# Kernel optimization log

Measured on AMD Instinct MI355X. Metric: run time of the kernel, lower is better.

The kernel has to match this reference:

```python
import jax, jax.numpy as jnp
import numpy as np
from jax import lax

# Mamba2 config (matches init_kwargs + mamba_ssm defaults)
B_SZ, SEQ = 8, 2048
D_MODEL, D_STATE, EXPAND, HEADDIM = 1024, 128, 2, 64
D_INNER = EXPAND * D_MODEL            # 2048
NHEADS = D_INNER // HEADDIM           # 32
NGROUPS, D_CONV, CHUNK = 1, 4, 128
CONV_DIM = D_INNER + 2 * NGROUPS * D_STATE
D_IN_PROJ = 2 * D_INNER + 2 * NGROUPS * D_STATE + NHEADS
VAR_NUM, EPS = 3, 1e-5


def setup_inputs() -> dict:
    key = jax.random.key(0)
    ks = jax.random.split(key, 10)
    return {
        "embed_data": jax.random.normal(ks[0], (B_SZ, SEQ, D_MODEL), jnp.float32),
        "in_proj_w": jax.random.normal(ks[1], (D_IN_PROJ, D_MODEL), jnp.float32) * 0.02,
        "conv_w": jax.random.normal(ks[2], (CONV_DIM, D_CONV), jnp.float32) * 0.2,
        "conv_b": jnp.zeros((CONV_DIM,), jnp.float32),
        "dt_bias": jnp.log(jnp.expm1(jax.random.uniform(ks[3], (NHEADS,), jnp.float32, 1e-3, 0.1))),
        "A_log": jnp.log(jax.random.uniform(ks[4], (NHEADS,), jnp.float32, 1.0, 16.0)),
        "D": jnp.ones((NHEADS,), jnp.float32),
        "norm_w": jnp.ones((D_INNER,), jnp.float32),
        "out_proj_w": jax.random.normal(ks[5], (D_MODEL, D_INNER), jnp.float32) * 0.02,
        "dec_w": jax.random.normal(ks[6], (VAR_NUM, D_MODEL), jnp.float32) * 0.02,
        "dec_b": jnp.zeros((VAR_NUM,), jnp.float32),
    }


def _segsum(a):
    # a: (b,h,c,L) -> (b,h,c,L,L) lower-triangular segment sums
    L = a.shape[-1]
    cs = jnp.cumsum(a, -1)
    ss = cs[..., :, None] - cs[..., None, :]
    mask = jnp.tril(jnp.ones((L, L), bool))
    return jnp.where(mask, ss, -jnp.inf)


def _ssd(x, dt, A, Bm, Cm):
    # x:(b,l,h,p) dt:(b,l,h) A:(h,) Bm,Cm:(b,l,n); chunked SSD scan (Mamba2)
    b, l, h, p = x.shape
    n = Bm.shape[-1]
    c = l // CHUNK
    xc = x.reshape(b, c, CHUNK, h, p)
    dtc = dt.reshape(b, c, CHUNK, h)
    Bc = Bm.reshape(b, c, CHUNK, n)
    Cc = Cm.reshape(b, c, CHUNK, n)
    ac = (dt * A).reshape(b, c, CHUNK, h).transpose(0, 3, 1, 2)  # (b,h,c,L)
    acs = jnp.cumsum(ac, -1)
    Lmat = jnp.exp(_segsum(ac))                                   # (b,h,c,L,L)
    xdt = xc * dtc[..., None]
    # intra-chunk (diagonal block) outputs
    CB = jnp.einsum('bcln,bcsn->bcls', Cc, Bc)
    Y_diag = jnp.einsum('bcls,bhcls,bcshp->bclhp', CB, Lmat, xdt)
    # per-chunk final states
    decay_states = jnp.exp(acs[..., -1:] - acs)                   # (b,h,c,L)
    states = jnp.einsum('bcln,bhcl,bclhp->bchpn', Bc, decay_states, xdt)
    chunk_decay = jnp.exp(acs[..., -1])                           # (b,h,c)
    def step(carry, inp):
        st, dec = inp
        return carry * dec[..., None, None] + st, carry
    _, states_in = lax.scan(step, jnp.zeros((b, h, p, n), x.dtype),
                            (jnp.moveaxis(states, 1, 0), jnp.moveaxis(chunk_decay, 2, 0)))
    states_in = jnp.moveaxis(states_in, 0, 1)                     # (b,c,h,p,n)
    # inter-chunk (off-diagonal) contribution
    Y_off = jnp.einsum('bcln,bchpn,bhcl->bclhp', Cc, states_in, jnp.exp(acs))
    return (Y_diag + Y_off).reshape(b, l, h, p)


def reference(embed_data, in_proj_w, conv_w, conv_b, dt_bias, A_log, D, norm_w, out_proj_w, dec_w, dec_b):
    b, l, _ = embed_data.shape
    zxbcdt = embed_data @ in_proj_w.T                             # (b,l,D_IN_PROJ)
    z = zxbcdt[..., :D_INNER]
    xBC = zxbcdt[..., D_INNER:D_INNER + CONV_DIM]
    dt = jax.nn.softplus(zxbcdt[..., D_INNER + CONV_DIM:] + dt_bias)  # (b,l,h)
    # causal depthwise conv1d + SiLU
    xt = lax.conv_general_dilated(xBC.transpose(0, 2, 1), conv_w[:, None, :], (1,),
                                  [(D_CONV - 1, 0)], feature_group_count=CONV_DIM,
                                  dimension_numbers=('NCH', 'OIH', 'NCH'))
    xBC = jax.nn.silu(xt.transpose(0, 2, 1) + conv_b)
    x = xBC[..., :D_INNER].reshape(b, l, NHEADS, HEADDIM)
    Bm = xBC[..., D_INNER:D_INNER + D_STATE]
    Cm = xBC[..., D_INNER + D_STATE:]
    A = -jnp.exp(A_log)
    y = _ssd(x, dt, A, Bm, Cm) + D[None, None, :, None] * x
    # gated RMSNorm
    y = y.reshape(b, l, D_INNER) * jax.nn.silu(z)
    y = y * lax.rsqrt(jnp.mean(y * y, -1, keepdims=True) + EPS) * norm_w
    hidden = y @ out_proj_w.T
    pred = hidden @ dec_w.T + dec_b
    return pred, hidden
```

## Files before the change

kernel.cpp:

```cpp
#include <hip/hip_runtime.h>
#include <cstdint>

#define DEVI __device__ __forceinline__

typedef unsigned short u16;
typedef unsigned int u32;
typedef __attribute__((ext_vector_type(4))) float f32x4;
typedef __attribute__((ext_vector_type(8))) u16 u16x8;
typedef __attribute__((ext_vector_type(4))) u16 u16x4;
typedef __attribute__((ext_vector_type(8))) __bf16 bf16x8;

#define SEQL 2048
#define NBATCH 8
#define MROWS (NBATCH*SEQL)
#define DMODEL 1024
#define DINNER 2048
#define NHEADS 32
#define HEADD 64
#define DSTATE 128
#define CONVD 2304
#define NPROJ 4384
#define NPROJP 4608
#define CHUNKL 128
#define NCHUNK 16
#define PADC 136

DEVI float bf2f(u16 v){ u32 u = ((u32)v)<<16; return __builtin_bit_cast(float,u); }
DEVI u16 f2bf(float f){ u32 u = __builtin_bit_cast(u32,f); u32 r = (u + 0x7fffu + ((u>>16)&1u))>>16; return (u16)r; }

DEVI void gld_lds16(const void* g, void* lds){
  __builtin_amdgcn_global_load_lds(
    (const __attribute__((address_space(1))) void*)(uintptr_t)g,
    (__attribute__((address_space(3))) void*)(u32)(uintptr_t)lds, 16, 0, 0);
}

DEVI f32x4 MFMA(u16x8 a, u16x8 b, f32x4 c){
  return __builtin_amdgcn_mfma_f32_16x16x32_bf16(
      __builtin_bit_cast(bf16x8,a), __builtin_bit_cast(bf16x8,b), c, 0,0,0);
}

__global__ void k_sentinel(float* o){ o[0] = 12345.0f; }

__global__ __launch_bounds__(256) void k_cvt(const float* __restrict__ src, u16* __restrict__ dst, long n, long ntot){
  long idx = ((long)blockIdx.x*256 + threadIdx.x)*4;
  if (idx >= ntot) return;
  u16x4 o;
  if (idx < n){
    f32x4 v = *(const f32x4*)(src+idx);
    o[0]=f2bf(v[0]); o[1]=f2bf(v[1]); o[2]=f2bf(v[2]); o[3]=f2bf(v[3]);
  } else { o[0]=0; o[1]=0; o[2]=0; o[3]=0; }
  *(u16x4*)(dst+idx) = o;
}

#define STG(mat, h, ts) do { \
    const int d_ = (ts) & 1; \
    const size_t ko_ = (size_t)(((ts) < NT) ? (ts) : (NT-1)) * 64; \
    gld_lds16(sbase[mat][h][0] + ko_, (char*)lds + (mat)*65536 + (d_*2+(h))*16384 + tid*16); \
    gld_lds16(sbase[mat][h][1] + ko_, (char*)lds + (mat)*65536 + (d_*2+(h))*16384 + 8192 + tid*16); \
  } while(0)

#define LDA8(AF, d_, qm) { \
    _Pragma("unroll") for (int mf=0; mf<4; mf++) \
    _Pragma("unroll") for (int ks=0; ks<2; ks++) \
      AF[mf][ks] = *(const u16x8*)(lds + (size_t)((d_)*2+wm)*8192 + ((qm)*64+mf*16+lidx)*64 + ((ks*4+krow)^(lidx&7))*8); }

#define LDB4(BF, d_, qn) { \
    _Pragma("unroll") for (int nf=0; nf<2; nf++) \
    _Pragma("unroll") for (int ks=0; ks<2; ks++) \
      BF[nf][ks] = *(const u16x8*)(lds + 32768 + (size_t)((d_)*2+(wn>>1))*8192 + ((wn&1)*64+(qn)*32+nf*16+lidx)*64 + ((ks*4+krow)^(lidx&7))*8); }

#define MMAQ(QM, QN, AF, BF) { \
    _Pragma("unroll") for (int mf=0; mf<4; mf++) \
    _Pragma("unroll") for (int nf=0; nf<2; nf++) \
    _Pragma("unroll") for (int ks=0; ks<2; ks++) \
      acc[(QM)*4+mf][(QN)*2+nf] = MFMA(AF[mf][ks], BF[nf][ks], acc[(QM)*4+mf][(QN)*2+nf]); }

#define BAR1 __builtin_amdgcn_sched_barrier(0); __builtin_amdgcn_s_barrier(); \
    asm volatile("s_waitcnt lgkmcnt(0)" ::: "memory"); __builtin_amdgcn_sched_barrier(0); \
    __builtin_amdgcn_s_setprio(1);
#define BAR2 __builtin_amdgcn_s_setprio(0); __builtin_amdgcn_sched_barrier(0); \
    __builtin_amdgcn_s_barrier(); __builtin_amdgcn_sched_barrier(0);

template<int MODE>
__global__ __launch_bounds__(512, 2) void k_gemm8(const u16* __restrict__ A, const u16* __restrict__ Bt,
    const int K, const int Ndim, float* __restrict__ outF,
    u16* __restrict__ z_out, u16* __restrict__ xbc_out, float* __restrict__ dtraw_out)
{
  extern __shared__ u16 lds[];
  const int NT = K >> 6;
  const int tid = threadIdx.x;
  const int lane = tid & 63, wid = tid >> 6;
  const int wm = wid >> 2, wn = wid & 3;
  const int lidx = lane & 15, krow = lane >> 4;
  const int nmt = gridDim.x, nnt = gridDim.y;
  const int nwg = nmt * nnt;
  const int orig = blockIdx.y * nmt + blockIdx.x;
  const int qq = nwg >> 3, rr = nwg & 7;
  const int xcd = orig & 7, li = orig >> 3;
  const int pid = (xcd < rr ? xcd*(qq+1) : rr*(qq+1) + (xcd-rr)*qq) + li;
  const int GM = 8;
  const int npg = GM * nnt;
  const int gid = pid / npg;
  const int rem = pid % npg;
  const int m0 = (gid*GM + (rem & (GM-1))) * 256;
  const int n0 = (rem / GM) * 256;

  f32x4 acc[8][4];
  const f32x4 zf = {0.f,0.f,0.f,0.f};
  #pragma unroll
  for (int i=0;i<8;i++)
    #pragma unroll
    for (int j=0;j<4;j++) acc[i][j] = zf;

  const int r0 = tid >> 3;
  const int gsw = ((tid & 7) ^ (r0 & 7)) * 8;
  const u16* sbase[2][2][2];
  #pragma unroll
  for (int h=0; h<2; h++)
    #pragma unroll
    for (int L=0; L<2; L++){
      sbase[0][h][L] = A  + (size_t)(m0 + h*128 + L*64 + r0)*K + gsw;
      sbase[1][h][L] = Bt + (size_t)(n0 + h*128 + L*64 + r0)*K + gsw;
    }

  STG(0,0,0); STG(0,1,0); STG(1,0,0); STG(1,1,0);
  asm volatile("s_waitcnt vmcnt(4)" ::: "memory");
  STG(0,0,1); STG(0,1,1); STG(1,0,1);
  asm volatile("s_waitcnt vmcnt(6)" ::: "memory");
  __builtin_amdgcn_sched_barrier(0);
  __builtin_amdgcn_s_barrier();
  __builtin_amdgcn_sched_barrier(0);

  u16x8 af[4][2], bf0[2][2], bf1[2][2];
  for (int t = 0; t < NT; t += 2){
    LDA8(af, 0, 0); LDB4(bf0, 0, 0); STG(1,1,t+1);
    BAR1; MMAQ(0,0,af,bf0); BAR2;
    LDB4(bf1, 0, 1);
    BAR1; MMAQ(0,1,af,bf1); BAR2;
    LDA8(af, 0, 1); STG(1,0,t+2);
    BAR1; MMAQ(1,1,af,bf1); BAR2;
    STG(0,0,t+2); STG(0,1,t+2);
    asm volatile("s_waitcnt vmcnt(6)" ::: "memory");
    BAR1; MMAQ(1,0,af,bf0); BAR2;
    LDA8(af, 1, 0); LDB4(bf0, 1, 0); STG(1,1,t+2);
    BAR1; MMAQ(0,0,af,bf0); BAR2;
    LDB4(bf1, 1, 1);
    BAR1; MMAQ(0,1,af,bf1); BAR2;
    LDA8(af, 1, 1); STG(1,0,t+3);
    BAR1; MMAQ(1,1,af,bf1); BAR2;
    STG(0,0,t+3); STG(0,1,t+3);
    asm volatile("s_waitcnt vmcnt(6)" ::: "memory");
    BAR1; MMAQ(1,0,af,bf0); BAR2;
  }
  asm volatile("s_waitcnt vmcnt(0)" ::: "memory");

  #pragma unroll
  for (int im=0; im<8; im++)
    #pragma unroll
    for (int in=0; in<4; in++)
      #pragma unroll
      for (int r=0; r<4; r++){
        int gm = m0 + wm*128 + im*16 + krow*4 + r;
        int gn = n0 + wn*64 + in*16 + lidx;
        float v = acc[im][in][r];
        if (MODE==0){
          outF[(long)gm*Ndim + gn] = v;
        } else {
          if (gn < DINNER) z_out[(long)gm*DINNER + gn] = f2bf(v);
          else if (gn < DINNER+CONVD) xbc_out[(long)gm*CONVD + (gn-DINNER)] = f2bf(v);
          else if (gn < NPROJ) dtraw_out[(long)gm*NHEADS + (gn-DINNER-CONVD)] = v;
        }
      }
}

__global__ __launch_bounds__(128) void k_dtprep(const float* __restrict__ dtraw, const float* __restrict__ dt_bias,
    const float* __restrict__ A_log, float* __restrict__ dt_t, float* __restrict__ acs_t)
{
  int b = blockIdx.x >> 9;
  int h = (blockIdx.x >> 4) & 31;
  int c = blockIdx.x & 15;
  int l = threadIdx.x;
  int gl = c*128 + l;
  float raw = dtraw[((long)(b*SEQL + gl))*NHEADS + h] + dt_bias[h];
  float dt = (raw > 20.f) ? raw : log1pf(expf(raw));
  float A = -expf(A_log[h]);
  float ac = dt*A;
  __shared__ float ss[128];
  ss[l] = ac; __syncthreads();
  for (int o=1;o<128;o<<=1){
    float v = (l>=o)? ss[l-o] : 0.f;
    __syncthreads();
    ss[l] += v;
    __syncthreads();
  }
  float acs = ss[l];
  dt_t[((long)(b*NHEADS+h))*SEQL + gl] = dt;
  acs_t[((long)(b*NHEADS+h))*SEQL + gl] = acs;
}

__global__ __launch_bounds__(256) void k_conv(const u16* __restrict__ xbc, const float* __restrict__ conv_w,
    const float* __restrict__ conv_b, const float* __restrict__ dt_t,
    u16* __restrict__ xdtT, u16* __restrict__ BTt, u16* __restrict__ CTt)
{
  __shared__ u16 sm[131*64];
  int idx = blockIdx.x;
  int b = idx / 576; int rem = idx % 576; int cbk = rem >> 4; int lb = rem & 15;
  int ch0 = cbk*64, l0 = lb*128;
  for (int g = threadIdx.x; g < 131*8; g += 256){
    int r = g >> 3, cg = g & 7;
    int gl = l0 - 3 + r;
    u16x8 v;
    if (gl >= 0) v = *(const u16x8*)(xbc + ((long)(b*SEQL+gl))*CONVD + ch0 + cg*8);
    else { v[0]=0;v[1]=0;v[2]=0;v[3]=0;v[4]=0;v[5]=0;v[6]=0;v[7]=0; }
    *(u16x8*)(&sm[r*64 + cg*8]) = v;
  }
  __syncthreads();
  int ci = threadIdx.x & 63, g4 = threadIdx.x >> 6;
  int chg = ch0 + ci;
  f32x4 wv = *(const f32x4*)(conv_w + chg*4);
  float bia = conv_b[chg];
  bool isX = chg < DINNER;
  int h = chg >> 6; if (h > 31) h = 31;
  int p = chg & 63;
  const float* dtrow = dt_t + ((long)(b*NHEADS+h))*SEQL + l0 + g4*32;
  u16x8 ov[4];
  #pragma unroll
  for (int i=0;i<32;i++){
    int lr = g4*32 + i;
    float a = bia + wv[0]*bf2f(sm[(lr+0)*64+ci]) + wv[1]*bf2f(sm[(lr+1)*64+ci])
                  + wv[2]*bf2f(sm[(lr+2)*64+ci]) + wv[3]*bf2f(sm[(lr+3)*64+ci]);
    float s = a / (1.f + __expf(-a));
    if (isX) s *= dtrow[i];
    ov[i>>3][i&7] = f2bf(s);
  }
  u16* dst;
  if (isX)                      dst = xdtT + (((long)(b*NHEADS+h))*HEADD + p)*SEQL + l0 + g4*32;
  else if (chg < DINNER+DSTATE) dst = BTt + ((long)(b*DSTATE + (chg-DINNER)))*SEQL + l0 + g4*32;
  else                          dst = CTt + ((long)(b*DSTATE + (chg-DINNER-DSTATE)))*SEQL + l0 + g4*32;
  #pragma unroll
  for (int q=0;q<4;q++) *(u16x8*)(dst + q*8) = ov[q];
}

__global__ __launch_bounds__(256) void k_cb(const u16* __restrict__ BTt, const u16* __restrict__ CTt,
      u16* __restrict__ CBm, u16* __restrict__ Cn)
{
  __shared__ u16 Cl[128*136];
  __shared__ u16 Bl[128*136];
  int b = blockIdx.x >> 4, c = blockIdx.x & 15;
  for (int g = threadIdx.x; g < 2048; g += 256){
    int n = g >> 4, lg = g & 15;
    u16x8 vc = *(const u16x8*)(CTt + ((long)(b*DSTATE+n))*SEQL + c*CHUNKL + lg*8);
    u16x8 vb = *(const u16x8*)(BTt + ((long)(b*DSTATE+n))*SEQL + c*CHUNKL + lg*8);
    #pragma unroll
    for (int j=0;j<8;j++){
      Cl[(lg*8+j)*136 + n] = vc[j];
      Bl[(lg*8+j)*136 + n] = vb[j];
    }
  }
  __syncthreads();
  const int tid = threadIdx.x;
  const int lane = tid & 63, wid = tid >> 6;
  const int wr = wid & 1, wc2 = wid >> 1;
  const int lidx = lane & 15, krow = lane >> 4;
  const f32x4 zf = {0.f,0.f,0.f,0.f};
  f32x4 acc[4][4];
  #pragma unroll
  for (int i=0;i<4;i++)
    #pragma unroll
    for (int j=0;j<4;j++) acc[i][j] = zf;
  #pragma unroll
  for (int k0=0;k0<128;k0+=32){
    u16x8 af[4], bfv[4];
    #pragma unroll
    for (int i=0;i<4;i++){
      af[i]  = *(const u16x8*)(&Cl[(wr*64+i*16+lidx)*136 + k0 + krow*8]);
      bfv[i] = *(const u16x8*)(&Bl[(wc2*64+i*16+lidx)*136 + k0 + krow*8]);
    }
    #pragma unroll
    for (int i=0;i<4;i++)
      #pragma unroll
      for (int j=0;j<4;j++)
        acc[i][j] = MFMA(af[i], bfv[j], acc[i][j]);
  }
  long base = ((long)(b*16+c))*128*128;
  #pragma unroll
  for (int i=0;i<4;i++)
    #pragma unroll
    for (int j=0;j<4;j++)
      #pragma unroll
      for (int r=0;r<4;r++){
        int l = wr*64+i*16+krow*4+r;
        int s = wc2*64+j*16+lidx;
        CBm[base + (long)l*128 + s] = f2bf(acc[i][j][r]);
      }
  for (int g = tid; g < 2048; g += 256){
    int l = g >> 4, ng = g & 15;
    u16x8 o;
    #pragma unroll
    for (int j=0;j<8;j++) o[j] = Cl[l*136 + ng*8 + j];
    *(u16x8*)(Cn + ((long)(b*SEQL + c*CHUNKL + l))*DSTATE + ng*8) = o;
  }
}

__global__ __launch_bounds__(256) void k_par(
    const u16* __restrict__ BTt, const u16* __restrict__ xdtT,
    const float* __restrict__ acs_t, u16* __restrict__ states)
{
  __shared__ u16 Bs[128*PADC];
  __shared__ u16 Xs[64*PADC];
  __shared__ float acs_s[128], dec_s[128];
  const int idx = blockIdx.x;
  const int c = idx & 15, bh = idx >> 4, b = bh >> 5;
  const int tid = threadIdx.x, lane = tid & 63, wid = tid >> 6;
  const int lidx = lane & 15, krow = lane >> 4;
  const int wps = wid & 1, wns = wid >> 1;
  const float* acs_g = acs_t + (long)bh*SEQL + c*128;
  const u16* X_g = xdtT + (long)bh*HEADD*SEQL + c*128;
  const u16* B_g = BTt + (long)b*DSTATE*SEQL + c*128;
  if (tid < 128) acs_s[tid] = acs_g[tid];
  __syncthreads();
  if (tid < 128) dec_s[tid] = __expf(acs_s[127] - acs_s[tid]);
  __syncthreads();
  for (int g = tid; g < 2048; g += 256){
    int n = g >> 4, lg = g & 15;
    u16x8 v = *(const u16x8*)(B_g + (long)n*SEQL + lg*8);
    u16x8 o;
    #pragma unroll
    for (int j=0;j<8;j++) o[j] = f2bf(bf2f(v[j])*dec_s[lg*8+j]);
    *(u16x8*)(&Bs[n*PADC + lg*8]) = o;
  }
  for (int g = tid; g < 1024; g += 256){
    int p = g >> 4, lg = g & 15;
    *(u16x8*)(&Xs[p*PADC + lg*8]) = *(const u16x8*)(X_g + (long)p*SEQL + lg*8);
  }
  __syncthreads();
  const f32x4 zf = {0.f,0.f,0.f,0.f};
  f32x4 accS[2][4];
  #pragma unroll
  for (int i=0;i<2;i++){ accS[i][0]=zf; accS[i][1]=zf; accS[i][2]=zf; accS[i][3]=zf; }
  #pragma unroll
  for (int k0=0;k0<128;k0+=32){
    u16x8 as2[2], bs2[4];
    #pragma unroll
    for (int i=0;i<2;i++) as2[i] = *(const u16x8*)(&Xs[(wps*32+i*16+lidx)*PADC + k0 + krow*8]);
    #pragma unroll
    for (int j=0;j<4;j++) bs2[j] = *(const u16x8*)(&Bs[(wns*64+j*16+lidx)*PADC + k0 + krow*8]);
    #pragma unroll
    for (int i=0;i<2;i++)
      #pragma unroll
      for (int j=0;j<4;j++)
        accS[i][j] = MFMA(as2[i], bs2[j], accS[i][j]);
  }
  u16* Sg = states + (long)idx*8192;
  #pragma unroll
  for (int i=0;i<2;i++)
    #pragma unroll
    for (int j=0;j<4;j++)
      #pragma unroll
      for (int r=0;r<4;r++){
        int p = wps*32 + i*16 + krow*4 + r;
        int n = wns*64 + j*16 + lidx;
        Sg[p*128 + n] = f2bf(accS[i][j][r]);
      }
}

__global__ __launch_bounds__(256) void k_scan(u16* __restrict__ states, const float* __restrict__ acs_t)
{
  long gid = (long)blockIdx.x*256 + threadIdx.x;
  int bh = (int)(gid >> 11);
  int q = (int)(gid & 2047);
  __shared__ float cds[16];
  if (threadIdx.x < 16) cds[threadIdx.x] = __expf(acs_t[(long)bh*SEQL + threadIdx.x*128 + 127]);
  __syncthreads();
  u16* p = states + (long)bh*NCHUNK*8192 + q*4;
  u16x4 sv[16];
  #pragma unroll
  for (int c=0;c<16;c++) sv[c] = *(const u16x4*)(p + c*8192);
  float c0=0.f,c1=0.f,c2=0.f,c3=0.f;
  #pragma unroll
  for (int c=0;c<16;c++){
    u16x4 o; o[0]=f2bf(c0); o[1]=f2bf(c1); o[2]=f2bf(c2); o[3]=f2bf(c3);
    *(u16x4*)(p + c*8192) = o;
    float cd = cds[c];
    c0 = c0*cd + bf2f(sv[c][0]);
    c1 = c1*cd + bf2f(sv[c][1]);
    c2 = c2*cd + bf2f(sv[c][2]);
    c3 = c3*cd + bf2f(sv[c][3]);
  }
}

__global__ __launch_bounds__(256) void k_yoff(
    const u16* __restrict__ Cng, const u16* __restrict__ xdtT, const u16* __restrict__ CBm,
    const u16* __restrict__ SI, const float* __restrict__ acs_t, const float* __restrict__ dt_t,
    const float* __restrict__ Dparam, u16* __restrict__ y)
{
  __shared__ u16 Ts[128*PADC];
  __shared__ u16 Us[64*PADC];
  __shared__ float acs_s[128], dtr_s[128], eacs_s[128];
  const int idx = blockIdx.x;
  const int c = idx & 15, bh = idx >> 4, b = bh >> 5, h = bh & 31;
  const int tid = threadIdx.x, lane = tid & 63, wid = tid >> 6;
  const int lidx = lane & 15, krow = lane >> 4;
  const int wl = wid & 1, wp = wid >> 1;
  const float Dh = Dparam[h];
  const float* acs_g = acs_t + (long)bh*SEQL + c*128;
  const float* dt_g  = dt_t  + (long)bh*SEQL + c*128;
  const u16* X_g = xdtT + (long)bh*HEADD*SEQL + c*128;
  const u16* C_g = Cng + ((long)(b*SEQL + c*128))*DSTATE;
  const u16* CB_g = CBm + ((long)(b*NCHUNK + c))*CHUNKL*CHUNKL;
  const u16* SI_g = SI + (long)idx*8192;
  if (tid < 128){ acs_s[tid] = acs_g[tid]; dtr_s[tid] = dt_g[tid]; }
  __syncthreads();
  if (tid < 128) eacs_s[tid] = __expf(acs_s[tid]);
  __syncthreads();
  {
    int l = tid >> 1, s0 = (tid & 1)*64;
    float al = acs_s[l];
    #pragma unroll
    for (int qq=0;qq<8;qq++){
      u16x8 v = *(const u16x8*)(CB_g + (long)l*CHUNKL + s0 + qq*8);
      u16x8 o;
      #pragma unroll
      for (int j=0;j<8;j++){
        int s = s0 + qq*8 + j;
        float pv = (s <= l) ? bf2f(v[j]) * __expf(al - acs_s[s]) : 0.f;
        o[j] = f2bf(pv);
      }
      *(u16x8*)(&Ts[l*PADC + s0 + qq*8]) = o;
    }
  }
  for (int g = tid; g < 1024; g += 256){
    int p = g >> 4, lg = g & 15;
    *(u16x8*)(&Us[p*PADC + lg*8]) = *(const u16x8*)(X_g + (long)p*SEQL + lg*8);
  }
  __syncthreads();
  const f32x4 zf = {0.f,0.f,0.f,0.f};
  f32x4 accY[4][2];
  #pragma unroll
  for (int i=0;i<4;i++){ accY[i][0]=zf; accY[i][1]=zf; }
  #pragma unroll
  for (int k0=0;k0<128;k0+=32){
    u16x8 af[4], bfv[2];
    #pragma unroll
    for (int i=0;i<4;i++) af[i] = *(const u16x8*)(&Ts[(wl*64+i*16+lidx)*PADC + k0 + krow*8]);
    #pragma unroll
    for (int j=0;j<2;j++) bfv[j] = *(const u16x8*)(&Us[(wp*32+j*16+lidx)*PADC + k0 + krow*8]);
    #pragma unroll
    for (int i=0;i<4;i++)
      #pragma unroll
      for (int j=0;j<2;j++)
        accY[i][j] = MFMA(af[i], bfv[j], accY[i][j]);
  }
  #pragma unroll
  for (int i=0;i<4;i++)
    #pragma unroll
    for (int j=0;j<2;j++)
      #pragma unroll
      for (int r=0;r<4;r++){
        int l = wl*64 + i*16 + krow*4 + r;
        int p = wp*32 + j*16 + lidx;
        accY[i][j][r] += Dh * bf2f(Us[p*PADC + l]) / dtr_s[l];
      }
  __syncthreads();
  for (int g = tid; g < 2048; g += 256){
    int l = g >> 4, cb = g & 15;
    u16x8 v = *(const u16x8*)(C_g + (long)l*DSTATE + cb*8);
    float e = eacs_s[l];
    u16x8 o;
    #pragma unroll
    for (int j=0;j<8;j++) o[j] = f2bf(bf2f(v[j])*e);
    *(u16x8*)(&Ts[l*PADC + cb*8]) = o;
  }
  for (int g = tid; g < 1024; g += 256){
    int p = g >> 4, lg = g & 15;
    *(u16x8*)(&Us[p*PADC + lg*8]) = *(const u16x8*)(SI_g + p*128 + lg*8);
  }
  __syncthreads();
  #pragma unroll
  for (int k0=0;k0<128;k0+=32){
    u16x8 af[4], bfv[2];
    #pragma unroll
    for (int i=0;i<4;i++) af[i] = *(const u16x8*)(&Ts[(wl*64+i*16+lidx)*PADC + k0 + krow*8]);
    #pragma unroll
    for (int j=0;j<2;j++) bfv[j] = *(const u16x8*)(&Us[(wp*32+j*16+lidx)*PADC + k0 + krow*8]);
    #pragma unroll
    for (int i=0;i<4;i++)
      #pragma unroll
      for (int j=0;j<2;j++)
        accY[i][j] = MFMA(af[i], bfv[j], accY[i][j]);
  }
  #pragma unroll
  for (int i=0;i<4;i++)
    #pragma unroll
    for (int j=0;j<2;j++)
      #pragma unroll
      for (int r=0;r<4;r++){
        int l = wl*64 + i*16 + krow*4 + r;
        int p = wp*32 + j*16 + lidx;
        y[((long)(b*SEQL + c*128 + l))*DINNER + h*HEADD + p] = f2bf(accY[i][j][r]);
      }
}

__global__ __launch_bounds__(256) void k_ssd(
    const u16* __restrict__ Cng, const u16* __restrict__ BTt, const u16* __restrict__ xdtT,
    const u16* __restrict__ CBm, const float* __restrict__ acs_t, const float* __restrict__ dt_t,
    const float* __restrict__ Dparam, u16* __restrict__ y)
{
  __shared__ u16 Cs[128*PADC];
  __shared__ u16 Bs[128*PADC];
  __shared__ u16 Ps[128*PADC];
  __shared__ u16 Xs[64*PADC];
  __shared__ float carry[64*132];
  __shared__ float acs_s[128], eacs_s[128], dec_s[128], dtr_s[128];
  const int bh = blockIdx.x;
  const int b = bh >> 5, h = bh & 31;
  const int tid = threadIdx.x, lane = tid & 63, wid = tid >> 6;
  const int lidx = lane & 15, krow = lane >> 4;
  const int wl = wid & 1, wp = wid >> 1;
  const int wps = wid & 1, wns = wid >> 1;
  for (int i = tid; i < 64*132; i += 256) carry[i] = 0.f;
  const float Dh = Dparam[h];
  const float* acs_g = acs_t + (long)bh*SEQL;
  const float* dt_g = dt_t + (long)bh*SEQL;
  const u16* X_g = xdtT + (long)bh*HEADD*SEQL;
  const u16* B_g = BTt + (long)b*DSTATE*SEQL;
  const u16* C_g = Cng + (long)b*SEQL*DSTATE;
  const u16* CB_g = CBm + (long)b*NCHUNK*CHUNKL*CHUNKL;
  const f32x4 zf = {0.f,0.f,0.f,0.f};
  for (int c=0;c<NCHUNK;c++){
    __syncthreads();
    if (tid < 128){ acs_s[tid] = acs_g[c*128+tid]; dtr_s[tid] = dt_g[c*128+tid]; }
    __syncthreads();
    if (tid < 128){ float a = acs_s[tid]; eacs_s[tid] = __expf(a); dec_s[tid] = __expf(acs_s[127]-a); }
    __syncthreads();
    for (int g = tid; g < 2048; g += 256){
      int l = g >> 4, cb = g & 15;
      u16x8 v = *(const u16x8*)(C_g + ((long)(c*128+l))*DSTATE + cb*8);
      float e = eacs_s[l];
      u16x8 o;
      #pragma unroll
      for (int j=0;j<8;j++) o[j] = f2bf(bf2f(v[j])*e);
      *(u16x8*)(&Cs[l*PADC + cb*8]) = o;
    }
    for (int g = tid; g < 2048; g += 256){
      int n = g >> 4, lg = g & 15;
      u16x8 v = *(const u16x8*)(B_g + (long)n*SEQL + c*128 + lg*8);
      u16x8 o;
      #pragma unroll
      for (int j=0;j<8;j++) o[j] = f2bf(bf2f(v[j])*dec_s[lg*8+j]);
      *(u16x8*)(&Bs[n*PADC + lg*8]) = o;
    }
    for (int g = tid; g < 1024; g += 256){
      int p = g >> 4, lg = g & 15;
      *(u16x8*)(&Xs[p*PADC + lg*8]) = *(const u16x8*)(X_g + (long)p*SEQL + c*128 + lg*8);
    }
    {
      int l = tid >> 1, s0 = (tid & 1)*64;
      float al = acs_s[l];
      #pragma unroll
      for (int q=0;q<8;q++){
        u16x8 v = *(const u16x8*)(CB_g + ((long)(c*128+l))*CHUNKL + s0 + q*8);
        u16x8 o;
        #pragma unroll
        for (int j=0;j<8;j++){
          int s = s0 + q*8 + j;
          float pv = (s <= l) ? bf2f(v[j]) * __expf(al - acs_s[s]) : 0.f;
          o[j] = f2bf(pv);
        }
        *(u16x8*)(&Ps[l*PADC + s0 + q*8]) = o;
      }
    }
    __syncthreads();
    f32x4 accY[4][2];
    f32x4 accS[2][4];
    #pragma unroll
    for (int i=0;i<4;i++){ accY[i][0]=zf; accY[i][1]=zf; }
    #pragma unroll
    for (int i=0;i<2;i++){ accS[i][0]=zf; accS[i][1]=zf; accS[i][2]=zf; accS[i][3]=zf; }
    #pragma unroll
    for (int k0=0;k0<128;k0+=32){
      u16x8 af[4], bfv[2];
      #pragma unroll
      for (int i=0;i<4;i++) af[i] = *(const u16x8*)(&Cs[(wl*64+i*16+lidx)*PADC + k0 + krow*8]);
      #pragma unroll
      for (int j=0;j<2;j++){
        const float* cp = &carry[(wp*32+j*16+lidx)*132 + k0 + krow*8];
        f32x4 c0 = *(const f32x4*)cp;
        f32x4 c1 = *(const f32x4*)(cp+4);
        u16x8 o;
        o[0]=f2bf(c0[0]); o[1]=f2bf(c0[1]); o[2]=f2bf(c0[2]); o[3]=f2bf(c0[3]);
        o[4]=f2bf(c1[0]); o[5]=f2bf(c1[1]); o[6]=f2bf(c1[2]); o[7]=f2bf(c1[3]);
        bfv[j] = o;
      }
      #pragma unroll
      for (int i=0;i<4;i++)
        #pragma unroll
        for (int j=0;j<2;j++)
          accY[i][j] = MFMA(af[i], bfv[j], accY[i][j]);
    }
    #pragma unroll
    for (int k0=0;k0<128;k0+=32){
      u16x8 af[4], bfv[2];
      #pragma unroll
      for (int i=0;i<4;i++) af[i] = *(const u16x8*)(&Ps[(wl*64+i*16+lidx)*PADC + k0 + krow*8]);
      #pragma unroll
      for (int j=0;j<2;j++) bfv[j] = *(const u16x8*)(&Xs[(wp*32+j*16+lidx)*PADC + k0 + krow*8]);
      #pragma unroll
      for (int i=0;i<4;i++)
        #pragma unroll
        for (int j=0;j<2;j++)
          accY[i][j] = MFMA(af[i], bfv[j], accY[i][j]);
    }
    #pragma unroll
    for (int k0=0;k0<128;k0+=32){
      u16x8 as2[2], bs2[4];
      #pragma unroll
      for (int i=0;i<2;i++) as2[i] = *(const u16x8*)(&Xs[(wps*32+i*16+lidx)*PADC + k0 + krow*8]);
      #pragma unroll
      for (int j=0;j<4;j++) bs2[j] = *(const u16x8*)(&Bs[(wns*64+j*16+lidx)*PADC + k0 + krow*8]);
      #pragma unroll
      for (int i=0;i<2;i++)
        #pragma unroll
        for (int j=0;j<4;j++)
          accS[i][j] = MFMA(as2[i], bs2[j], accS[i][j]);
    }
    __syncthreads();
    float cd = __expf(acs_s[127]);
    #pragma unroll
    for (int i=0;i<2;i++)
      #pragma unroll
      for (int j=0;j<4;j++)
        #pragma unroll
        for (int r=0;r<4;r++){
          int p = wps*32 + i*16 + krow*4 + r;
          int n = wns*64 + j*16 + lidx;
          carry[p*132+n] = carry[p*132+n]*cd + accS[i][j][r];
        }
    #pragma unroll
    for (int i=0;i<4;i++)
      #pragma unroll
      for (int j=0;j<2;j++)
        #pragma unroll
        for (int r=0;r<4;r++){
          int l = wl*64 + i*16 + krow*4 + r;
          int p = wp*32 + j*16 + lidx;
          float xv = bf2f(Xs[p*PADC + l]) / dtr_s[l];
          float val = accY[i][j][r] + Dh*xv;
          y[((long)(b*SEQL + c*128 + l))*DINNER + h*HEADD + p] = f2bf(val);
        }
  }
}

__global__ __launch_bounds__(256) void k_gate(const u16* __restrict__ y, const u16* __restrict__ z,
    const float* __restrict__ norm_w, u16* __restrict__ out)
{
  long row = blockIdx.x;
  const u16* yr = y + row*DINNER;
  const u16* zr = z + row*DINNER;
  int t = threadIdx.x;
  u16x8 yy = *(const u16x8*)(yr + t*8);
  u16x8 zz = *(const u16x8*)(zr + t*8);
  float g[8]; float ss = 0.f;
  #pragma unroll
  for (int j=0;j<8;j++){
    float zfv = bf2f(zz[j]);
    float sg = zfv / (1.f + __expf(-zfv));
    float gv = bf2f(yy[j]) * sg;
    g[j] = gv; ss += gv*gv;
  }
  #pragma unroll
  for (int o=32;o>0;o>>=1) ss += __shfl_down(ss, o);
  __shared__ float part[4];
  int lane = t & 63, wid = t>>6;
  if (lane==0) part[wid] = ss;
  __syncthreads();
  float tot = part[0]+part[1]+part[2]+part[3];
  float inv = rsqrtf(tot*(1.f/DINNER) + 1e-5f);
  u16x8 o;
  #pragma unroll
  for (int j=0;j<8;j++) o[j] = f2bf(g[j]*inv*norm_w[t*8+j]);
  *(u16x8*)(out + row*DINNER + t*8) = o;
}

__global__ __launch_bounds__(256) void k_pred(const float* __restrict__ hid, const float* __restrict__ dec_w,
    const float* __restrict__ dec_b, float* __restrict__ pred)
{
  int t = threadIdx.x;
  long row = (long)blockIdx.x*8 + (t>>5);
  int lk = t & 31;
  const float* hr = hid + row*DMODEL;
  float a0=0.f,a1=0.f,a2=0.f;
  #pragma unroll
  for (int i=0;i<8;i++){
    f32x4 hv = *(const f32x4*)(hr + lk*4 + i*128);
    f32x4 w0 = *(const f32x4*)(dec_w + 0*DMODEL + lk*4 + i*128);
    f32x4 w1 = *(const f32x4*)(dec_w + 1*DMODEL + lk*4 + i*128);
    f32x4 w2 = *(const f32x4*)(dec_w + 2*DMODEL + lk*4 + i*128);
    a0 += hv[0]*w0[0]+hv[1]*w0[1]+hv[2]*w0[2]+hv[3]*w0[3];
    a1 += hv[0]*w1[0]+hv[1]*w1[1]+hv[2]*w1[2]+hv[3]*w1[3];
    a2 += hv[0]*w2[0]+hv[1]*w2[1]+hv[2]*w2[2]+hv[3]*w2[3];
  }
  #pragma unroll
  for (int o=16;o>0;o>>=1){
    a0 += __shfl_down(a0,o,32); a1 += __shfl_down(a1,o,32); a2 += __shfl_down(a2,o,32);
  }
  if (lk==0){
    pred[row*3+0] = a0 + dec_b[0];
    pred[row*3+1] = a1 + dec_b[1];
    pred[row*3+2] = a2 + dec_b[2];
  }
}

extern "C" void kernel_launch(void* const* d_in, const int* in_sizes, int n_in,
                              void* d_out, int out_size, void* d_ws, size_t ws_size,
                              hipStream_t stream)
{
  const float* embed      = (const float*)d_in[0];
  const float* in_proj_w  = (const float*)d_in[1];
  const float* conv_w     = (const float*)d_in[2];
  const float* conv_b     = (const float*)d_in[3];
  const float* dt_bias    = (const float*)d_in[4];
  const float* A_log      = (const float*)d_in[5];
  const float* Dp         = (const float*)d_in[6];
  const float* norm_w     = (const float*)d_in[7];
  const float* out_proj_w = (const float*)d_in[8];
  const float* dec_w      = (const float*)d_in[9];
  const float* dec_b      = (const float*)d_in[10];

  char* ws = (char*)d_ws;
  size_t off = 0;
  auto alloc = [&](size_t bytes)->void*{ void* p = ws + off; off += (bytes + 255) & ~(size_t)255; return p; };

  u16* xbc = (u16*)alloc((size_t)MROWS*CONVD*2);
  u16* yb  = xbc;
  u16* R2  = (u16*)alloc((size_t)MROWS*DINNER*2);
  u16* Ebf = R2;
  u16* W1  = R2 + (size_t)MROWS*DMODEL;
  u16* xdtT  = R2;
  u16* ynorm = R2;
  float* dtraw = (float*)alloc((size_t)MROWS*NHEADS*4);
  float* dt_t  = (float*)alloc((size_t)NBATCH*NHEADS*SEQL*4);
  float* acs   = (float*)alloc((size_t)NBATCH*NHEADS*SEQL*4);
  u16* BTt   = (u16*)alloc((size_t)NBATCH*DSTATE*SEQL*2);
  u16* CTt   = (u16*)alloc((size_t)NBATCH*DSTATE*SEQL*2);
  u16* Cn    = (u16*)alloc((size_t)NBATCH*SEQL*DSTATE*2);
  u16* CBm   = (u16*)alloc((size_t)NBATCH*NCHUNK*CHUNKL*CHUNKL*2);
  u16* W2    = (u16*)alloc((size_t)DMODEL*DINNER*2);

  size_t off_base = off;
  u16* S = (u16*)alloc((size_t)NBATCH*NHEADS*NCHUNK*HEADD*DSTATE*2);
  bool use_par = (off <= ws_size);

  if (off_base > ws_size){
    k_sentinel<<<1,1,0,stream>>>((float*)d_out);
    return;
  }

  float* pred   = (float*)d_out;
  float* hidden = (float*)d_out + (size_t)MROWS*3;
  u16* zb = (u16*)hidden;

  hipFuncSetAttribute((const void*)k_gemm8<1>, hipFuncAttributeMaxDynamicSharedMemorySize, 131072);
  hipFuncSetAttribute((const void*)k_gemm8<0>, hipFuncAttributeMaxDynamicSharedMemorySize, 131072);

  k_cvt<<<16384,256,0,stream>>>(embed, Ebf, (long)MROWS*DMODEL, (long)MROWS*DMODEL);
  k_cvt<<<4608,256,0,stream>>>(in_proj_w, W1, (long)NPROJ*DMODEL, (long)NPROJP*DMODEL);
  k_cvt<<<2048,256,0,stream>>>(out_proj_w, W2, (long)DMODEL*DINNER, (long)DMODEL*DINNER);
  {
    dim3 g1(64, NPROJP/256);
    k_gemm8<1><<<g1,512,131072,stream>>>(Ebf, W1, DMODEL, 0, nullptr, zb, xbc, dtraw);
  }
  k_dtprep<<<4096,128,0,stream>>>(dtraw, dt_bias, A_log, dt_t, acs);
  k_conv<<<4608,256,0,stream>>>(xbc, conv_w, conv_b, dt_t, xdtT, BTt, CTt);
  k_cb<<<128,256,0,stream>>>(BTt, CTt, CBm, Cn);
  if (use_par){
    k_par<<<4096,256,0,stream>>>(BTt, xdtT, acs, S);
    k_scan<<<2048,256,0,stream>>>(S, acs);
    k_yoff<<<4096,256,0,stream>>>(Cn, xdtT, CBm, S, acs, dt_t, Dp, yb);
  } else {
    k_ssd<<<256,256,0,stream>>>(Cn, BTt, xdtT, CBm, acs, dt_t, Dp, yb);
  }
  k_gate<<<16384,256,0,stream>>>(yb, zb, norm_w, ynorm);
  {
    dim3 g2(64, DMODEL/256);
    k_gemm8<0><<<g2,512,131072,stream>>>(ynorm, W2, DINNER, DMODEL, hidden, nullptr, nullptr, nullptr);
  }
  k_pred<<<2048,256,0,stream>>>(hidden, dec_w, dec_b, pred);
}
```

Measured before the change: 533.9 us.

## Merge conversion launches and fuse CB with chunk-state kernel; add LDS wait hint

After: 532.1 us. About the same (-0.3%).

```diff
diff --git a/kernel.cpp b/kernel.cpp
--- a/kernel.cpp
+++ b/kernel.cpp
@@ -41,9 +41,16 @@
 
 __global__ void k_sentinel(float* o){ o[0] = 12345.0f; }
 
-__global__ __launch_bounds__(256) void k_cvt(const float* __restrict__ src, u16* __restrict__ dst, long n, long ntot){
-  long idx = ((long)blockIdx.x*256 + threadIdx.x)*4;
-  if (idx >= ntot) return;
+__global__ __launch_bounds__(256) void k_cvt3(const float* __restrict__ e, u16* __restrict__ eb,
+    const float* __restrict__ w1, u16* __restrict__ w1b,
+    const float* __restrict__ w2, u16* __restrict__ w2b)
+{
+  int bid = blockIdx.x;
+  const float* src; u16* dst; long n; long base;
+  if (bid < 16384){ src = e;  dst = eb;  n = (long)MROWS*DMODEL;  base = (long)bid*1024; }
+  else if (bid < 20992){ src = w1; dst = w1b; n = (long)NPROJ*DMODEL; base = (long)(bid-16384)*1024; }
+  else { src = w2; dst = w2b; n = (long)DMODEL*DINNER; base = (long)(bid-20992)*1024; }
+  long idx = base + (long)threadIdx.x*4;
   u16x4 o;
   if (idx < n){
     f32x4 v = *(const f32x4*)(src+idx);
@@ -74,6 +81,8 @@
     _Pragma("unroll") for (int nf=0; nf<2; nf++) \
     _Pragma("unroll") for (int ks=0; ks<2; ks++) \
       acc[(QM)*4+mf][(QN)*2+nf] = MFMA(AF[mf][ks], BF[nf][ks], acc[(QM)*4+mf][(QN)*2+nf]); }
+
+#define LHINT asm volatile("s_waitcnt lgkmcnt(8)" ::: "memory");
 
 #define BAR1 __builtin_amdgcn_sched_barrier(0); __builtin_amdgcn_s_barrier(); \
     asm volatile("s_waitcnt lgkmcnt(0)" ::: "memory"); __builtin_amdgcn_sched_barrier(0); \
@@ -133,7 +142,7 @@
 
   u16x8 af[4][2], bf0[2][2], bf1[2][2];
   for (int t = 0; t < NT; t += 2){
-    LDA8(af, 0, 0); LDB4(bf0, 0, 0); STG(1,1,t+1);
+    LDA8(af, 0, 0); LDB4(bf0, 0, 0); STG(1,1,t+1); LHINT;
     BAR1; MMAQ(0,0,af,bf0); BAR2;
     LDB4(bf1, 0, 1);
     BAR1; MMAQ(0,1,af,bf1); BAR2;
@@ -142,7 +151,7 @@
     STG(0,0,t+2); STG(0,1,t+2);
     asm volatile("s_waitcnt vmcnt(6)" ::: "memory");
     BAR1; MMAQ(1,0,af,bf0); BAR2;
-    LDA8(af, 1, 0); LDB4(bf0, 1, 0); STG(1,1,t+2);
+    LDA8(af, 1, 0); LDB4(bf0, 1, 0); STG(1,1,t+2); LHINT;
     BAR1; MMAQ(0,0,af,bf0); BAR2;
     LDB4(bf1, 1, 1);
     BAR1; MMAQ(0,1,af,bf1); BAR2;
@@ -241,127 +250,124 @@
   for (int q=0;q<4;q++) *(u16x8*)(dst + q*8) = ov[q];
 }
 
-__global__ __launch_bounds__(256) void k_cb(const u16* __restrict__ BTt, const u16* __restrict__ CTt,
-      u16* __restrict__ CBm, u16* __restrict__ Cn)
-{
-  __shared__ u16 Cl[128*136];
-  __shared__ u16 Bl[128*136];
-  int b = blockIdx.x >> 4, c = blockIdx.x & 15;
-  for (int g = threadIdx.x; g < 2048; g += 256){
-    int n = g >> 4, lg = g & 15;
-    u16x8 vc = *(const u16x8*)(CTt + ((long)(b*DSTATE+n))*SEQL + c*CHUNKL + lg*8);
-    u16x8 vb = *(const u16x8*)(BTt + ((long)(b*DSTATE+n))*SEQL + c*CHUNKL + lg*8);
-    #pragma unroll
-    for (int j=0;j<8;j++){
-      Cl[(lg*8+j)*136 + n] = vc[j];
-      Bl[(lg*8+j)*136 + n] = vb[j];
-    }
-  }
-  __syncthreads();
+__global__ __launch_bounds__(256) void k_cbpar(const u16* __restrict__ BTt, const u16* __restrict__ CTt,
+    const u16* __restrict__ xdtT, const float* __restrict__ acs_t,
+    u16* __restrict__ CBm, u16* __restrict__ Cn, u16* __restrict__ states)
+{
+  __shared__ __align__(16) char smem[69632];
   const int tid = threadIdx.x;
   const int lane = tid & 63, wid = tid >> 6;
-  const int wr = wid & 1, wc2 = wid >> 1;
   const int lidx = lane & 15, krow = lane >> 4;
   const f32x4 zf = {0.f,0.f,0.f,0.f};
-  f32x4 acc[4][4];
-  #pragma unroll
-  for (int i=0;i<4;i++)
-    #pragma unroll
-    for (int j=0;j<4;j++) acc[i][j] = zf;
-  #pragma unroll
-  for (int k0=0;k0<128;k0+=32){
-    u16x8 af[4], bfv[4];
-    #pragma unroll
-    for (int i=0;i<4;i++){
-      af[i]  = *(const u16x8*)(&Cl[(wr*64+i*16+lidx)*136 + k0 + krow*8]);
-      bfv[i] = *(const u16x8*)(&Bl[(wc2*64+i*16+lidx)*136 + k0 + krow*8]);
-    }
+  if (blockIdx.x < 128){
+    u16* Cl = (u16*)smem;
+    u16* Bl = (u16*)(smem + 34816);
+    int b = blockIdx.x >> 4, c = blockIdx.x & 15;
+    for (int g = tid; g < 2048; g += 256){
+      int n = g >> 4, lg = g & 15;
+      u16x8 vc = *(const u16x8*)(CTt + ((long)(b*DSTATE+n))*SEQL + c*CHUNKL + lg*8);
+      u16x8 vb = *(const u16x8*)(BTt + ((long)(b*DSTATE+n))*SEQL + c*CHUNKL + lg*8);
+      #pragma unroll
+      for (int j=0;j<8;j++){
+        Cl[(lg*8+j)*136 + n] = vc[j];
+        Bl[(lg*8+j)*136 + n] = vb[j];
+      }
+    }
+    __syncthreads();
+    const int wr = wid & 1, wc2 = wid >> 1;
+    f32x4 acc[4][4];
     #pragma unroll
     for (int i=0;i<4;i++)
       #pragma unroll
+      for (int j=0;j<4;j++) acc[i][j] = zf;
+    #pragma unroll
+    for (int k0=0;k0<128;k0+=32){
+      u16x8 af[4], bfv[4];
+      #pragma unroll
+      for (int i=0;i<4;i++){
+        af[i]  = *(const u16x8*)(&Cl[(wr*64+i*16+lidx)*136 + k0 + krow*8]);
+        bfv[i] = *(const u16x8*)(&Bl[(wc2*64+i*16+lidx)*136 + k0 + krow*8]);
+      }
+      #pragma unroll
+      for (int i=0;i<4;i++)
+        #pragma unroll
+        for (int j=0;j<4;j++)
+          acc[i][j] = MFMA(af[i], bfv[j], acc[i][j]);
+    }
+    long base = ((long)(b*16+c))*128*128;
+    #pragma unroll
+    for (int i=0;i<4;i++)
+      #pragma unroll
       for (int j=0;j<4;j++)
-        acc[i][j] = MFMA(af[i], bfv[j], acc[i][j]);
-  }
-  long base = ((long)(b*16+c))*128*128;
-  #pragma unroll
-  for (int i=0;i<4;i++)
-    #pragma unroll
-    for (int j=0;j<4;j++)
-      #pragma unroll
-      for (int r=0;r<4;r++){
-        int l = wr*64+i*16+krow*4+r;
-        int s = wc2*64+j*16+lidx;
-        CBm[base + (long)l*128 + s] = f2bf(acc[i][j][r]);
-      }
-  for (int g = tid; g < 2048; g += 256){
-    int l = g >> 4, ng = g & 15;
-    u16x8 o;
-    #pragma unroll
-    for (int j=0;j<8;j++) o[j] = Cl[l*136 + ng*8 + j];
-    *(u16x8*)(Cn + ((long)(b*SEQL + c*CHUNKL + l))*DSTATE + ng*8) = o;
-  }
-}
-
-__global__ __launch_bounds__(256) void k_par(
-    const u16* __restrict__ BTt, const u16* __restrict__ xdtT,
-    const float* __restrict__ acs_t, u16* __restrict__ states)
-{
-  __shared__ u16 Bs[128*PADC];
-  __shared__ u16 Xs[64*PADC];
-  __shared__ float acs_s[128], dec_s[128];
-  const int idx = blockIdx.x;
-  const int c = idx & 15, bh = idx >> 4, b = bh >> 5;
-  const int tid = threadIdx.x, lane = tid & 63, wid = tid >> 6;
-  const int lidx = lane & 15, krow = lane >> 4;
-  const int wps = wid & 1, wns = wid >> 1;
-  const float* acs_g = acs_t + (long)bh*SEQL + c*128;
-  const u16* X_g = xdtT + (long)bh*HEADD*SEQL + c*128;
-  const u16* B_g = BTt + (long)b*DSTATE*SEQL + c*128;
-  if (tid < 128) acs_s[tid] = acs_g[tid];
-  __syncthreads();
-  if (tid < 128) dec_s[tid] = __expf(acs_s[127] - acs_s[tid]);
-  __syncthreads();
-  for (int g = tid; g < 2048; g += 256){
-    int n = g >> 4, lg = g & 15;
-    u16x8 v = *(const u16x8*)(B_g + (long)n*SEQL + lg*8);
-    u16x8 o;
-    #pragma unroll
-    for (int j=0;j<8;j++) o[j] = f2bf(bf2f(v[j])*dec_s[lg*8+j]);
-    *(u16x8*)(&Bs[n*PADC + lg*8]) = o;
-  }
-  for (int g = tid; g < 1024; g += 256){
-    int p = g >> 4, lg = g & 15;
-    *(u16x8*)(&Xs[p*PADC + lg*8]) = *(const u16x8*)(X_g + (long)p*SEQL + lg*8);
-  }
-  __syncthreads();
-  const f32x4 zf = {0.f,0.f,0.f,0.f};
-  f32x4 accS[2][4];
-  #pragma unroll
-  for (int i=0;i<2;i++){ accS[i][0]=zf; accS[i][1]=zf; accS[i][2]=zf; accS[i][3]=zf; }
-  #pragma unroll
-  for (int k0=0;k0<128;k0+=32){
-    u16x8 as2[2], bs2[4];
-    #pragma unroll
-    for (int i=0;i<2;i++) as2[i] = *(const u16x8*)(&Xs[(wps*32+i*16+lidx)*PADC + k0 + krow*8]);
-    #pragma unroll
-    for (int j=0;j<4;j++) bs2[j] = *(const u16x8*)(&Bs[(wns*64+j*16+lidx)*PADC + k0 + krow*8]);
+        #pragma unroll
+        for (int r=0;r<4;r++){
+          int l = wr*64+i*16+krow*4+r;
+          int s = wc2*64+j*16+lidx;
+          CBm[base + (long)l*128 + s] = f2bf(acc[i][j][r]);
+        }
+    for (int g = tid; g < 2048; g += 256){
+      int l = g >> 4, ng = g & 15;
+      u16x8 o;
+      #pragma unroll
+      for (int j=0;j<8;j++) o[j] = Cl[l*136 + ng*8 + j];
+      *(u16x8*)(Cn + ((long)(b*SEQL + c*CHUNKL + l))*DSTATE + ng*8) = o;
+    }
+  } else {
+    u16* Bs = (u16*)smem;
+    u16* Xs = (u16*)(smem + 34816);
+    float* acs_s = (float*)(smem + 52224);
+    float* dec_s = (float*)(smem + 52736);
+    const int idx = blockIdx.x - 128;
+    const int c = idx & 15, bh = idx >> 4, b = bh >> 5;
+    const int wps = wid & 1, wns = wid >> 1;
+    const float* acs_g = acs_t + (long)bh*SEQL + c*128;
+    const u16* X_g = xdtT + (long)bh*HEADD*SEQL + c*128;
+    const u16* B_g = BTt + (long)b*DSTATE*SEQL + c*128;
+    if (tid < 128) acs_s[tid] = acs_g[tid];
+    __syncthreads();
+    if (tid < 128) dec_s[tid] = __expf(acs_s[127] - acs_s[tid]);
+    __syncthreads();
+    for (int g = tid; g < 2048; g += 256){
+      int n = g >> 4, lg = g & 15;
+      u16x8 v = *(const u16x8*)(B_g + (long)n*SEQL + lg*8);
+      u16x8 o;
+      #pragma unroll
+      for (int j=0;j<8;j++) o[j] = f2bf(bf2f(v[j])*dec_s[lg*8+j]);
+      *(u16x8*)(&Bs[n*PADC + lg*8]) = o;
+    }
+    for (int g = tid; g < 1024; g += 256){
+      int p = g >> 4, lg = g & 15;
+      *(u16x8*)(&Xs[p*PADC + lg*8]) = *(const u16x8*)(X_g + (long)p*SEQL + lg*8);
+    }
+    __syncthreads();
+    f32x4 accS[2][4];
+    #pragma unroll
+    for (int i=0;i<2;i++){ accS[i][0]=zf; accS[i][1]=zf; accS[i][2]=zf; accS[i][3]=zf; }
+    #pragma unroll
+    for (int k0=0;k0<128;k0+=32){
+      u16x8 as2[2], bs2[4];
+      #pragma unroll
+      for (int i=0;i<2;i++) as2[i] = *(const u16x8*)(&Xs[(wps*32+i*16+lidx)*PADC + k0 + krow*8]);
+      #pragma unroll
+      for (int j=0;j<4;j++) bs2[j] = *(const u16x8*)(&Bs[(wns*64+j*16+lidx)*PADC + k0 + krow*8]);
+      #pragma unroll
+      for (int i=0;i<2;i++)
+        #pragma unroll
+        for (int j=0;j<4;j++)
+          accS[i][j] = MFMA(as2[i], bs2[j], accS[i][j]);
+    }
+    u16* Sg = states + (long)idx*8192;
     #pragma unroll
     for (int i=0;i<2;i++)
       #pragma unroll
       for (int j=0;j<4;j++)
-        accS[i][j] = MFMA(as2[i], bs2[j], accS[i][j]);
-  }
-  u16* Sg = states + (long)idx*8192;
-  #pragma unroll
-  for (int i=0;i<2;i++)
-    #pragma unroll
-    for (int j=0;j<4;j++)
-      #pragma unroll
-      for (int r=0;r<4;r++){
-        int p = wps*32 + i*16 + krow*4 + r;
-        int n = wns*64 + j*16 + lidx;
-        Sg[p*128 + n] = f2bf(accS[i][j][r]);
-      }
+        #pragma unroll
+        for (int r=0;r<4;r++){
+          int p = wps*32 + i*16 + krow*4 + r;
+          int n = wns*64 + j*16 + lidx;
+          Sg[p*128 + n] = f2bf(accS[i][j][r]);
+        }
+  }
 }
 
 __global__ __launch_bounds__(256) void k_scan(u16* __restrict__ states, const float* __restrict__ acs_t)
@@ -763,18 +769,15 @@
   hipFuncSetAttribute((const void*)k_gemm8<1>, hipFuncAttributeMaxDynamicSharedMemorySize, 131072);
   hipFuncSetAttribute((const void*)k_gemm8<0>, hipFuncAttributeMaxDynamicSharedMemorySize, 131072);
 
-  k_cvt<<<16384,256,0,stream>>>(embed, Ebf, (long)MROWS*DMODEL, (long)MROWS*DMODEL);
-  k_cvt<<<4608,256,0,stream>>>(in_proj_w, W1, (long)NPROJ*DMODEL, (long)NPROJP*DMODEL);
-  k_cvt<<<2048,256,0,stream>>>(out_proj_w, W2, (long)DMODEL*DINNER, (long)DMODEL*DINNER);
+  k_cvt3<<<23040,256,0,stream>>>(embed, Ebf, in_proj_w, W1, out_proj_w, W2);
   {
     dim3 g1(64, NPROJP/256);
     k_gemm8<1><<<g1,512,131072,stream>>>(Ebf, W1, DMODEL, 0, nullptr, zb, xbc, dtraw);
   }
   k_dtprep<<<4096,128,0,stream>>>(dtraw, dt_bias, A_log, dt_t, acs);
   k_conv<<<4608,256,0,stream>>>(xbc, conv_w, conv_b, dt_t, xdtT, BTt, CTt);
-  k_cb<<<128,256,0,stream>>>(BTt, CTt, CBm, Cn);
+  k_cbpar<<<(use_par ? 4224 : 128),256,0,stream>>>(BTt, CTt, xdtT, acs, CBm, Cn, S);
   if (use_par){
-    k_par<<<4096,256,0,stream>>>(BTt, xdtT, acs, S);
     k_scan<<<2048,256,0,stream>>>(S, acs);
     k_yoff<<<4096,256,0,stream>>>(Cn, xdtT, CBm, S, acs, dt_t, Dp, yb);
   } else {
```
